# Performance work log

Hardware: AMD Instinct MI355X
Metric: run time of the kernel (lower is better)

Reference implementation:

```python
import jax, jax.numpy as jnp
import numpy as np

INPUT_DIM = 29
OUTPUT_DIM = 67
ES = 256
HS = 512
SRC_LEN = 64
TRG_LEN = 48
BATCH = 512


def _lstm_cell(x, h, c, Wih, Whh, bih, bhh):
    # PyTorch gate order: i, f, g, o
    g = x @ Wih.T + bih + h @ Whh.T + bhh
    i, f, gg, o = jnp.split(g, 4, axis=-1)
    c_new = jax.nn.sigmoid(f) * c + jax.nn.sigmoid(i) * jnp.tanh(gg)
    h_new = jax.nn.sigmoid(o) * jnp.tanh(c_new)
    return h_new, c_new


def setup_inputs() -> dict:
    key = jax.random.key(0)
    ks = jax.random.split(key, 32)
    s_es = 1.0 / np.sqrt(ES)
    s_hs = 1.0 / np.sqrt(HS)
    inp = {}
    inp['src'] = jax.random.randint(ks[0], (SRC_LEN, BATCH), 0, INPUT_DIM)
    inp['trg'] = jax.random.randint(ks[1], (TRG_LEN, BATCH), 0, OUTPUT_DIM)
    # encoder params
    inp['enc_emb'] = jax.random.normal(ks[2], (INPUT_DIM, ES), jnp.float32)
    inp['enc_Wih_f'] = jax.random.normal(ks[3], (4 * HS, ES), jnp.float32) * s_hs
    inp['enc_Whh_f'] = jax.random.normal(ks[4], (4 * HS, HS), jnp.float32) * s_hs
    inp['enc_bih_f'] = jax.random.normal(ks[5], (4 * HS,), jnp.float32) * s_hs
    inp['enc_bhh_f'] = jax.random.normal(ks[6], (4 * HS,), jnp.float32) * s_hs
    inp['enc_Wih_b'] = jax.random.normal(ks[7], (4 * HS, ES), jnp.float32) * s_hs
    inp['enc_Whh_b'] = jax.random.normal(ks[8], (4 * HS, HS), jnp.float32) * s_hs
    inp['enc_bih_b'] = jax.random.normal(ks[9], (4 * HS,), jnp.float32) * s_hs
    inp['enc_bhh_b'] = jax.random.normal(ks[10], (4 * HS,), jnp.float32) * s_hs
    inp['fc_h_W'] = jax.random.normal(ks[11], (HS, 2 * HS), jnp.float32) * s_hs
    inp['fc_h_b'] = jax.random.normal(ks[12], (HS,), jnp.float32) * s_hs
    inp['fc_c_W'] = jax.random.normal(ks[13], (HS, 2 * HS), jnp.float32) * s_hs
    inp['fc_c_b'] = jax.random.normal(ks[14], (HS,), jnp.float32) * s_hs
    # decoder params
    inp['dec_emb'] = jax.random.normal(ks[15], (OUTPUT_DIM, ES), jnp.float32)
    inp['dec_Wih'] = jax.random.normal(ks[16], (4 * HS, 2 * HS + ES), jnp.float32) * s_hs
    inp['dec_Whh'] = jax.random.normal(ks[17], (4 * HS, HS), jnp.float32) * s_hs
    inp['dec_bih'] = jax.random.normal(ks[18], (4 * HS,), jnp.float32) * s_hs
    inp['dec_bhh'] = jax.random.normal(ks[19], (4 * HS,), jnp.float32) * s_hs
    inp['energy_W'] = jax.random.normal(ks[20], (1, 3 * HS), jnp.float32) * s_hs
    inp['energy_b'] = jax.random.normal(ks[21], (1,), jnp.float32) * s_hs
    inp['fc_out_W'] = jax.random.normal(ks[22], (OUTPUT_DIM, HS), jnp.float32) * s_hs
    inp['fc_out_b'] = jax.random.normal(ks[23], (OUTPUT_DIM,), jnp.float32) * s_hs
    return inp


def _forward(src, trg, enc_emb, enc_Wih_f, enc_Whh_f, enc_bih_f, enc_bhh_f,
             enc_Wih_b, enc_Whh_b, enc_bih_b, enc_bhh_b,
             fc_h_W, fc_h_b, fc_c_W, fc_c_b,
             dec_emb, dec_Wih, dec_Whh, dec_bih, dec_bhh,
             energy_W, energy_b, fc_out_W, fc_out_b):
    S, B = src.shape
    T = trg.shape[0]
    emb = enc_emb[src]  # [S, B, ES]
    h0 = jnp.zeros((B, HS), emb.dtype)
    c0 = jnp.zeros((B, HS), emb.dtype)

    def fwd_step(carry, x_t):
        h, c = carry
        h, c = _lstm_cell(x_t, h, c, enc_Wih_f, enc_Whh_f, enc_bih_f, enc_bhh_f)
        return (h, c), h

    def bwd_step(carry, x_t):
        h, c = carry
        h, c = _lstm_cell(x_t, h, c, enc_Wih_b, enc_Whh_b, enc_bih_b, enc_bhh_b)
        return (h, c), h

    (hf, cf), out_f = jax.lax.scan(fwd_step, (h0, c0), emb)
    (hb, cb), out_b_rev = jax.lax.scan(bwd_step, (h0, c0), emb[::-1])
    out_b = out_b_rev[::-1]
    encoder_states = jnp.concatenate([out_f, out_b], axis=2)  # [S, B, 2H]

    # fc_h / fc_c compress the 2 directions' final hidden/cell to [B, H]
    hidden_h = jnp.concatenate([hf, hb], axis=-1) @ fc_h_W.T + fc_h_b
    hidden_c = jnp.concatenate([cf, cb], axis=-1) @ fc_c_W.T + fc_c_b

    # Attention: original code passes encoder_hidden on EVERY step, so the
    # attention weights and context vector are constant across decode steps.
    h_rep = jnp.broadcast_to(hidden_h[None], (S, B, HS))
    e_in = jnp.concatenate([h_rep, encoder_states], axis=2)  # [S, B, 3H]
    energy = jax.nn.relu(e_in @ energy_W.T + energy_b)  # [S, B, 1]
    attn = jax.nn.softmax(energy, axis=0)[..., 0]  # [S, B]
    context = jnp.einsum('sb,sbh->bh', attn, encoder_states)  # [B, 2H]

    # Decode: teacher_forcing_ratio = 1.0 -> inputs are trg[t-1]; since the
    # rnn initial state is reset to encoder_hidden each step, all T-1 steps
    # are independent and can be computed in parallel.
    dec_in_tok = trg[:-1]  # [T-1, B]
    emb_d = dec_emb[dec_in_tok]  # [T-1, B, ES]
    ctx_rep = jnp.broadcast_to(context[None], (T - 1, B, 2 * HS))
    rnn_in = jnp.concatenate([ctx_rep, emb_d], axis=2)  # [T-1, B, 2H+ES]
    h_new, _ = _lstm_cell(rnn_in, hidden_h[None], hidden_c[None],
                          dec_Wih, dec_Whh, dec_bih, dec_bhh)
    logits = h_new @ fc_out_W.T + fc_out_b  # [T-1, B, V]
    outputs = jnp.concatenate(
        [jnp.zeros((1, B, OUTPUT_DIM), logits.dtype), logits], axis=0)
    return outputs


def reference(src, trg, enc_emb, enc_Wih_f, enc_Whh_f, enc_bih_f, enc_bhh_f,
              enc_Wih_b, enc_Whh_b, enc_bih_b, enc_bhh_b,
              fc_h_W, fc_h_b, fc_c_W, fc_c_b,
              dec_emb, dec_Wih, dec_Whh, dec_bih, dec_bhh,
              energy_W, energy_b, fc_out_W, fc_out_b):
    return _forward(src, trg, enc_emb, enc_Wih_f, enc_Whh_f, enc_bih_f,
                    enc_bhh_f, enc_Wih_b, enc_Whh_b, enc_bih_b, enc_bhh_b,
                    fc_h_W, fc_h_b, fc_c_W, fc_c_b, dec_emb, dec_Wih,
                    dec_Whh, dec_bih, dec_bhh, energy_W, energy_b,
                    fc_out_W, fc_out_b)
```

## Files before the change

kernel.cpp:

```cpp
#include <hip/hip_runtime.h>
#include <cstddef>

#define BATCH 512
#define ESZ   256
#define HSZ   512
#define G4    2048
#define SRCL  64
#define TRGL  48
#define ODIM  67

typedef __bf16  bf8v    __attribute__((ext_vector_type(8)));
typedef float   floatx4 __attribute__((ext_vector_type(4)));

__device__ __forceinline__ float frcp(float x) { return __builtin_amdgcn_rcpf(x); }
__device__ __forceinline__ float fsig(float x) { return frcp(1.0f + __expf(-x)); }
__device__ __forceinline__ float ftanh(float x) { return 1.0f - 2.0f * frcp(1.0f + __expf(2.0f * x)); }

__global__ void embed_bf16(const int* __restrict__ tok, const float* __restrict__ table,
                           __bf16* __restrict__ out, int n_rows) {
    int i = blockIdx.x * 256 + threadIdx.x;
    int row = i >> 5;
    if (row >= n_rows) return;
    int e = (i & 31) << 3;
    const float* src = table + (size_t)tok[row] * ESZ + e;
    float4 a = *(const float4*)src;
    float4 b = *(const float4*)(src + 4);
    bf8v v;
    v[0] = (__bf16)a.x; v[1] = (__bf16)a.y; v[2] = (__bf16)a.z; v[3] = (__bf16)a.w;
    v[4] = (__bf16)b.x; v[5] = (__bf16)b.y; v[6] = (__bf16)b.z; v[7] = (__bf16)b.w;
    *(bf8v*)(out + (size_t)row * ESZ + e) = v;
}

__global__ void zero_kernel(float* __restrict__ p, int n) {
    int i = blockIdx.x * 256 + threadIdx.x;
    if (i < n) p[i] = 0.f;
}

__global__ void bias_prep(const float* __restrict__ af, const float* __restrict__ bf,
                          const float* __restrict__ ab, const float* __restrict__ bb,
                          const float* __restrict__ ad, const float* __restrict__ bd,
                          float* __restrict__ of, float* __restrict__ ob, float* __restrict__ od) {
    int i = blockIdx.x * 256 + threadIdx.x;
    if (i < G4) { of[i] = af[i] + bf[i]; ob[i] = ab[i] + bb[i]; od[i] = ad[i] + bd[i]; }
}

__device__ __forceinline__ bf8v cvt8(const float* __restrict__ s) {
    float4 a = *(const float4*)s;
    float4 b = *(const float4*)(s + 4);
    bf8v v;
    v[0] = (__bf16)a.x; v[1] = (__bf16)a.y; v[2] = (__bf16)a.z; v[3] = (__bf16)a.w;
    v[4] = (__bf16)b.x; v[5] = (__bf16)b.y; v[6] = (__bf16)b.z; v[7] = (__bf16)b.w;
    return v;
}

__global__ void wcat_bf16(const float* __restrict__ Wih, const float* __restrict__ Whh,
                          __bf16* __restrict__ Wc) {
    int i = blockIdx.x * 256 + threadIdx.x;
    int n = i / 96;
    int e = (i - n * 96) << 3;
    const float* src = (e < ESZ) ? (Wih + (size_t)n * ESZ + e)
                                 : (Whh + (size_t)n * HSZ + (e - ESZ));
    *(bf8v*)(Wc + (size_t)n * 768 + e) = cvt8(src);
}

__global__ void decw_bf16(const float* __restrict__ dec_Wih, __bf16* __restrict__ We) {
    int i = blockIdx.x * 256 + threadIdx.x;
    int n = i >> 5;
    int e = (i & 31) << 3;
    *(bf8v*)(We + (size_t)n * ESZ + e) =
        cvt8(dec_Wih + (size_t)n * (2 * HSZ + ESZ) + 2 * HSZ + e);
}

__global__ void wdcat_bf16(const float* __restrict__ dec_Wih, const float* __restrict__ dec_Whh,
                           __bf16* __restrict__ Wd) {
    int i = blockIdx.x * 256 + threadIdx.x;
    int n = i / 192;
    int e = (i - n * 192) << 3;
    const float* src = (e < 1024) ? (dec_Wih + (size_t)n * 1280 + e)
                                  : (dec_Whh + (size_t)n * HSZ + (e - 1024));
    *(bf8v*)(Wd + (size_t)n * 1536 + e) = cvt8(src);
}

__global__ void conv_f2b(const float* __restrict__ src, __bf16* __restrict__ dst, int n8) {
    int i = blockIdx.x * 256 + threadIdx.x;
    if (i < n8) *(bf8v*)(dst + (size_t)i * 8) = cvt8(src + (size_t)i * 8);
}

__global__ void fo_pad(const float* __restrict__ W, __bf16* __restrict__ dst) {
    int i = blockIdx.x * 256 + threadIdx.x;
    int r = i >> 6, e = (i & 63) << 3;
    bf8v v;
    if (r < ODIM) v = cvt8(W + (size_t)r * HSZ + e);
    else { for (int k = 0; k < 8; ++k) v[k] = (__bf16)0.f; }
    *(bf8v*)(dst + (size_t)r * HSZ + e) = v;
}

__global__ void cat_hfb(const __bf16* __restrict__ es, __bf16* __restrict__ dst) {
    int i = blockIdx.x * 256 + threadIdx.x;
    int r = i >> 7, e = (i & 127) << 3;
    const __bf16* s = (e < HSZ) ? (es + ((size_t)(63 * BATCH + r)) * 1024 + e)
                                : (es + (size_t)r * 1024 + e);
    *(bf8v*)(dst + (size_t)r * 1024 + e) = *(const bf8v*)s;
}

__global__ void cat_cfb(const float* __restrict__ cbuf, __bf16* __restrict__ dst) {
    int i = blockIdx.x * 256 + threadIdx.x;
    int r = i >> 7, e = (i & 127) << 3;
    const float* s = (e < HSZ) ? (cbuf + (size_t)r * HSZ + e)
                               : (cbuf + (size_t)BATCH * HSZ + (size_t)r * HSZ + (e - HSZ));
    *(bf8v*)(dst + (size_t)r * 1024 + e) = cvt8(s);
}

__global__ void cat_ctxh(const float* __restrict__ ctx, const float* __restrict__ hid_h,
                         __bf16* __restrict__ dst) {
    int i = blockIdx.x * 256 + threadIdx.x;
    int r = i / 192;
    int e = (i - r * 192) << 3;
    const float* s = (e < 1024) ? (ctx + (size_t)r * 1024 + e)
                                : (hid_h + (size_t)r * HSZ + (e - 1024));
    *(bf8v*)(dst + (size_t)r * 1536 + e) = cvt8(s);
}

__global__ __launch_bounds__(256) void enc_step_v3(
    const __bf16* __restrict__ embE, const __bf16* __restrict__ hPrev,
    __bf16* __restrict__ hNext, float* __restrict__ cbuf, __bf16* __restrict__ es,
    const __bf16* __restrict__ WcF, const __bf16* __restrict__ WcB,
    const float* __restrict__ biasF, const float* __restrict__ biasB, int t)
{
    __shared__ __bf16 As[64 * 136];
    __shared__ __bf16 Bs[64 * 136];
    __shared__ float  gbuf[64 * 64];

    const int dir = blockIdx.z;
    const int tt  = dir ? (SRCL - 1 - t) : t;
    const __bf16* Wc   = dir ? WcB : WcF;
    const float*  bias = dir ? biasB : biasF;
    const int j0 = blockIdx.x * 16;
    const int m0 = blockIdx.y * 64;

    const int tid = threadIdx.x;
    const int w = tid >> 6, lane = tid & 63;
    const int quad = lane >> 4, l15 = lane & 15;
    const int mh = (w & 1) * 32, gh = (w >> 1) * 32;

    floatx4 acc[2][2] = {};

    for (int p = 0; p < 6; ++p) {
        __syncthreads();
#pragma unroll
        for (int i = 0; i < 4; ++i) {
            int idx = tid + i * 256;
            int r = idx >> 4, kq = idx & 15;
            const __bf16* srcA;
            if (p < 2) srcA = embE + ((size_t)(tt * BATCH + m0 + r)) * ESZ + p * 128 + kq * 8;
            else       srcA = hPrev + ((size_t)(dir * BATCH + m0 + r)) * HSZ + (p - 2) * 128 + kq * 8;
            *(bf8v*)(As + r * 136 + kq * 8) = *(const bf8v*)srcA;
            int wrow = (r >> 4) * HSZ + j0 + (r & 15);
            *(bf8v*)(Bs + r * 136 + kq * 8) =
                *(const bf8v*)(Wc + (size_t)wrow * 768 + p * 128 + kq * 8);
        }
        __syncthreads();
#pragma unroll
        for (int ks = 0; ks < 4; ++ks) {
            int ko = (ks * 4 + quad) * 8;
            bf8v a0 = *(const bf8v*)(As + (mh + l15) * 136 + ko);
            bf8v a1 = *(const bf8v*)(As + (mh + 16 + l15) * 136 + ko);
            bf8v b0 = *(const bf8v*)(Bs + (gh + l15) * 136 + ko);
            bf8v b1 = *(const bf8v*)(Bs + (gh + 16 + l15) * 136 + ko);
            acc[0][0] = __builtin_amdgcn_mfma_f32_16x16x32_bf16(a0, b0, acc[0][0], 0, 0, 0);
            acc[0][1] = __builtin_amdgcn_mfma_f32_16x16x32_bf16(a0, b1, acc[0][1], 0, 0, 0);
            acc[1][0] = __builtin_amdgcn_mfma_f32_16x16x32_bf16(a1, b0, acc[1][0], 0, 0, 0);
            acc[1][1] = __builtin_amdgcn_mfma_f32_16x16x32_bf16(a1, b1, acc[1][1], 0, 0, 0);
        }
    }

#pragma unroll
    for (int ms = 0; ms < 2; ++ms)
#pragma unroll
        for (int cs = 0; cs < 2; ++cs)
#pragma unroll
            for (int r = 0; r < 4; ++r)
                gbuf[(mh + ms * 16 + quad * 4 + r) * 64 + gh + cs * 16 + l15] = acc[ms][cs][r];
    __syncthreads();

#pragma unroll
    for (int i = 0; i < 4; ++i) {
        int e = tid + i * 256;
        int m = e >> 4, jj = e & 15;
        float gi = gbuf[m * 64 + jj]      + bias[j0 + jj];
        float gf = gbuf[m * 64 + 16 + jj] + bias[HSZ + j0 + jj];
        float gg = gbuf[m * 64 + 32 + jj] + bias[2 * HSZ + j0 + jj];
        float go = gbuf[m * 64 + 48 + jj] + bias[3 * HSZ + j0 + jj];
        size_t ci = (size_t)(dir * BATCH + m0 + m) * HSZ + j0 + jj;
        float cn = fsig(gf) * cbuf[ci] + fsig(gi) * ftanh(gg);
        cbuf[ci] = cn;
        float hn = fsig(go) * ftanh(cn);
        hNext[ci] = (__bf16)hn;
        es[((size_t)(tt * BATCH + m0 + m)) * (2 * HSZ) + dir * HSZ + j0 + jj] = (__bf16)hn;
    }
}

__global__ __launch_bounds__(256) void gmm_bf16(
    const __bf16* __restrict__ A, const __bf16* __restrict__ B, int K,
    const float* __restrict__ bias, float* __restrict__ C, int ldc, int N)
{
    const int tid = threadIdx.x;
    const int w = tid >> 6, lane = tid & 63;
    const int quad = lane >> 4, l15 = lane & 15;
    const int n0 = blockIdx.x * 64;
    const int mA = blockIdx.y * 64 + w * 16 + l15;

    const __bf16* Ar = A + (size_t)mA * K + quad * 8;
    const __bf16* Br[4];
#pragma unroll
    for (int ns = 0; ns < 4; ++ns)
        Br[ns] = B + (size_t)(n0 + ns * 16 + l15) * K + quad * 8;

    floatx4 acc[4] = {};
    const int KT = K >> 5;
#pragma unroll 4
    for (int kt = 0; kt < KT; ++kt) {
        bf8v a = *(const bf8v*)(Ar + kt * 32);
#pragma unroll
        for (int ns = 0; ns < 4; ++ns) {
            bf8v b = *(const bf8v*)(Br[ns] + kt * 32);
            acc[ns] = __builtin_amdgcn_mfma_f32_16x16x32_bf16(a, b, acc[ns], 0, 0, 0);
        }
    }
    const int mb = blockIdx.y * 64 + w * 16 + quad * 4;
#pragma unroll
    for (int ns = 0; ns < 4; ++ns) {
        int n = n0 + ns * 16 + l15;
        if (n < N) {
#pragma unroll
            for (int r = 0; r < 4; ++r)
                C[(size_t)(mb + r) * ldc + n] = acc[ns][r] + bias[n];
        }
    }
}

__global__ __launch_bounds__(256) void dec_mfma(
    const __bf16* __restrict__ embD, const __bf16* __restrict__ We,
    const float* __restrict__ D0, const float* __restrict__ hidc,
    __bf16* __restrict__ h_new)
{
    const int tid = threadIdx.x;
    const int w = tid >> 6, lane = tid & 63;
    const int quad = lane >> 4, l15 = lane & 15;
    const int mA = blockIdx.y * 64 + w * 16 + l15;
    const int j0 = blockIdx.x * 32;

    const __bf16* Ar = embD + (size_t)mA * ESZ + quad * 8;
    const __bf16* Brow[4][2];
#pragma unroll
    for (int g = 0; g < 4; ++g)
#pragma unroll
        for (int ni = 0; ni < 2; ++ni)
            Brow[g][ni] = We + ((size_t)(g * HSZ + j0 + ni * 16 + l15)) * ESZ + quad * 8;

    floatx4 acc[4][2] = {};
#pragma unroll 4
    for (int kt = 0; kt < 8; ++kt) {
        bf8v a = *(const bf8v*)(Ar + kt * 32);
#pragma unroll
        for (int g = 0; g < 4; ++g)
#pragma unroll
            for (int ni = 0; ni < 2; ++ni) {
                bf8v b = *(const bf8v*)(Brow[g][ni] + kt * 32);
                acc[g][ni] = __builtin_amdgcn_mfma_f32_16x16x32_bf16(a, b, acc[g][ni], 0, 0, 0);
            }
    }

    const int mbase = blockIdx.y * 64 + w * 16 + quad * 4;
#pragma unroll
    for (int ni = 0; ni < 2; ++ni) {
        int j = j0 + ni * 16 + l15;
#pragma unroll
        for (int r = 0; r < 4; ++r) {
            int mr = mbase + r;
            int b = mr & (BATCH - 1);
            const float* d0 = D0 + (size_t)b * G4;
            float gi = acc[0][ni][r] + d0[j];
            float gf = acc[1][ni][r] + d0[HSZ + j];
            float gg = acc[2][ni][r] + d0[2 * HSZ + j];
            float go = acc[3][ni][r] + d0[3 * HSZ + j];
            float cn = fsig(gf) * hidc[(size_t)b * HSZ + j] + fsig(gi) * ftanh(gg);
            h_new[(size_t)mr * HSZ + j] = (__bf16)(fsig(go) * ftanh(cn));
        }
    }
}

__global__ void eh_kernel(const float* __restrict__ hid_h, const float* __restrict__ eW,
                          const float* __restrict__ eb, float* __restrict__ eh) {
    int w = blockIdx.x * 4 + (threadIdx.x >> 6);
    int lane = threadIdx.x & 63;
    if (w >= BATCH) return;
    float s = 0.f;
    for (int k = lane; k < HSZ; k += 64) s += hid_h[(size_t)w * HSZ + k] * eW[k];
    for (int off = 32; off; off >>= 1) s += __shfl_down(s, off);
    if (lane == 0) eh[w] = s + eb[0];
}

__global__ void energy_kernel(const __bf16* __restrict__ es, const float* __restrict__ eW2,
                              const float* __restrict__ eh, float* __restrict__ energy) {
    int w = blockIdx.x * 4 + (threadIdx.x >> 6);
    int lane = threadIdx.x & 63;
    int s = w >> 9, b = w & 511;
    const __bf16* row = es + ((size_t)s * BATCH + b) * (2 * HSZ);
    float v = 0.f;
    for (int k = lane; k < 2 * HSZ; k += 64) v += (float)row[k] * eW2[k];
    for (int off = 32; off; off >>= 1) v += __shfl_down(v, off);
    if (lane == 0) energy[(size_t)s * BATCH + b] = fmaxf(v + eh[b], 0.f);
}

__global__ void softmax_kernel(const float* __restrict__ energy, float* __restrict__ attn) {
    int b = blockIdx.x * 4 + (threadIdx.x >> 6);
    int lane = threadIdx.x & 63;
    if (b >= BATCH) return;
    float v = energy[(size_t)lane * BATCH + b];
    float m = v;
    for (int off = 32; off; off >>= 1) m = fmaxf(m, __shfl_xor(m, off));
    float e = __expf(v - m);
    float sum = e;
    for (int off = 32; off; off >>= 1) sum += __shfl_xor(sum, off);
    attn[(size_t)lane * BATCH + b] = e / sum;
}

__global__ void context_kernel(const float* __restrict__ attn, const __bf16* __restrict__ es,
                               float* __restrict__ ctx) {
    int b = blockIdx.x;
    int j = threadIdx.x * 4;
    float a0 = 0.f, a1 = 0.f, a2 = 0.f, a3 = 0.f;
    for (int s = 0; s < SRCL; ++s) {
        float a = attn[(size_t)s * BATCH + b];
        const __bf16* r = es + ((size_t)s * BATCH + b) * (2 * HSZ) + j;
        a0 += a * (float)r[0]; a1 += a * (float)r[1];
        a2 += a * (float)r[2]; a3 += a * (float)r[3];
    }
    float4 o = make_float4(a0, a1, a2, a3);
    *(float4*)(ctx + (size_t)b * (2 * HSZ) + j) = o;
}

extern "C" void kernel_launch(void* const* d_in, const int* in_sizes, int n_in,
                              void* d_out, int out_size, void* d_ws, size_t ws_size,
                              hipStream_t stream) {
    const int*   src      = (const int*)d_in[0];
    const int*   trg      = (const int*)d_in[1];
    const float* enc_emb  = (const float*)d_in[2];
    const float* Wih_f    = (const float*)d_in[3];
    const float* Whh_f    = (const float*)d_in[4];
    const float* bih_f    = (const float*)d_in[5];
    const float* bhh_f    = (const float*)d_in[6];
    const float* Wih_b    = (const float*)d_in[7];
    const float* Whh_b    = (const float*)d_in[8];
    const float* bih_b    = (const float*)d_in[9];
    const float* bhh_b    = (const float*)d_in[10];
    const float* fc_h_W   = (const float*)d_in[11];
    const float* fc_h_b   = (const float*)d_in[12];
    const float* fc_c_W   = (const float*)d_in[13];
    const float* fc_c_b   = (const float*)d_in[14];
    const float* dec_emb  = (const float*)d_in[15];
    const float* dec_Wih  = (const float*)d_in[16];
    const float* dec_Whh  = (const float*)d_in[17];
    const float* dec_bih  = (const float*)d_in[18];
    const float* dec_bhh  = (const float*)d_in[19];
    const float* energy_W = (const float*)d_in[20];
    const float* energy_b = (const float*)d_in[21];
    const float* fc_out_W = (const float*)d_in[22];
    const float* fc_out_b = (const float*)d_in[23];
    float* out = (float*)d_out;

    float* ws = (float*)d_ws;
    size_t o = 0;
    __bf16* embE = (__bf16*)(ws + o); o += 4194304;
    __bf16* embD = (__bf16*)(ws + o); o += 3080192;
    __bf16* es   = (__bf16*)(ws + o); o += 16777216;
    float* zbase = ws + o;
    __bf16* h0   = (__bf16*)(ws + o); o += 262144;
    __bf16* h1   = (__bf16*)(ws + o); o += 262144;
    float*  cbuf = ws + o;            o += 524288;
    __bf16* WcF  = (__bf16*)(ws + o); o += 786432;
    __bf16* WcB  = (__bf16*)(ws + o); o += 786432;
    __bf16* decWe= (__bf16*)(ws + o); o += 262144;
    __bf16* WdC  = (__bf16*)(ws + o); o += 1572864;
    __bf16* fcWh = (__bf16*)(ws + o); o += 262144;
    __bf16* fcWc = (__bf16*)(ws + o); o += 262144;
    __bf16* foWb = (__bf16*)(ws + o); o += 32768;
    __bf16* hfb  = (__bf16*)(ws + o); o += 262144;
    __bf16* cfb  = (__bf16*)(ws + o); o += 262144;
    __bf16* ctxh = (__bf16*)(ws + o); o += 393216;
    float* hid_h = ws + o;            o += 262144;
    float* hid_c = ws + o;            o += 262144;
    float* ehv   = ws + o;            o += 512;
    float* energy= ws + o;            o += 32768;
    float* attn  = ws + o;            o += 32768;
    float* ctx   = ws + o;            o += 524288;
    float* D0    = ws + o;            o += 1048576;
    float* bias_f= ws + o;            o += 2048;
    float* bias_b= ws + o;            o += 2048;
    float* bias_d= ws + o;            o += 2048;
    __bf16* h_new= (__bf16*)(ws + o); o += 6160384;

    embed_bf16<<<4096, 256, 0, stream>>>(src, enc_emb, embE, SRCL * BATCH);
    embed_bf16<<<3008, 256, 0, stream>>>(trg, dec_emb, embD, (TRGL - 1) * BATCH);
    zero_kernel<<<4096, 256, 0, stream>>>(zbase, 1048576);
    bias_prep<<<8, 256, 0, stream>>>(bih_f, bhh_f, bih_b, bhh_b, dec_bih, dec_bhh,
                                     bias_f, bias_b, bias_d);
    wcat_bf16<<<768, 256, 0, stream>>>(Wih_f, Whh_f, WcF);
    wcat_bf16<<<768, 256, 0, stream>>>(Wih_b, Whh_b, WcB);
    decw_bf16<<<256, 256, 0, stream>>>(dec_Wih, decWe);
    wdcat_bf16<<<1536, 256, 0, stream>>>(dec_Wih, dec_Whh, WdC);
    conv_f2b<<<256, 256, 0, stream>>>(fc_h_W, fcWh, 65536);
    conv_f2b<<<256, 256, 0, stream>>>(fc_c_W, fcWc, 65536);
    fo_pad<<<32, 256, 0, stream>>>(fc_out_W, foWb);

    for (int t = 0; t < SRCL; ++t) {
        const __bf16* hp = (t & 1) ? h1 : h0;
        __bf16*       hn = (t & 1) ? h0 : h1;
        enc_step_v3<<<dim3(32, 8, 2), 256, 0, stream>>>(
            embE, hp, hn, cbuf, es, WcF, WcB, bias_f, bias_b, t);
    }

    cat_hfb<<<256, 256, 0, stream>>>(es, hfb);
    cat_cfb<<<256, 256, 0, stream>>>(cbuf, cfb);
    gmm_bf16<<<dim3(8, 8), 256, 0, stream>>>(hfb, fcWh, 1024, fc_h_b, hid_h, HSZ, HSZ);
    gmm_bf16<<<dim3(8, 8), 256, 0, stream>>>(cfb, fcWc, 1024, fc_c_b, hid_c, HSZ, HSZ);

    eh_kernel<<<128, 256, 0, stream>>>(hid_h, energy_W, energy_b, ehv);
    energy_kernel<<<8192, 256, 0, stream>>>(es, energy_W + HSZ, ehv, energy);
    softmax_kernel<<<128, 256, 0, stream>>>(energy, attn);
    context_kernel<<<512, 256, 0, stream>>>(attn, es, ctx);

    cat_ctxh<<<384, 256, 0, stream>>>(ctx, hid_h, ctxh);
    gmm_bf16<<<dim3(32, 8), 256, 0, stream>>>(ctxh, WdC, 1536, bias_d, D0, G4, G4);

    dec_mfma<<<dim3(16, 376), 256, 0, stream>>>(embD, decWe, D0, hid_c, h_new);

    zero_kernel<<<134, 256, 0, stream>>>(out, BATCH * ODIM);
    gmm_bf16<<<dim3(2, 376), 256, 0, stream>>>(h_new, foWb, HSZ, fc_out_b,
                                               out + (size_t)BATCH * ODIM, ODIM, ODIM);
}
```

Measured before the change: 1.315 ms.

## Fuse encoder timesteps into a persistent kernel with grid barriers; retile decoder

Replaces the 64 per-timestep encoder launches with one persistent kernel of 256 blocks. Each block keeps its slice of the recurrent weights resident in shared memory and synchronises only with the 16 blocks sharing its batch rows through atomic counters between timesteps. The decoder gate kernel is also retiled to 128-row tiles staged in LDS, reading a gate-interleaved copy of D0 produced by a new swizzle kernel. The persistent kernel removes launch overhead and repeated weight reloads, but it requires all 256 blocks to be co-resident (launch_bounds 256,1) and adds spin-wait barrier latency on every step.

```diff
diff --git a/kernel.cpp b/kernel.cpp
--- a/kernel.cpp
+++ b/kernel.cpp
@@ -11,6 +11,10 @@
 
 typedef __bf16  bf8v    __attribute__((ext_vector_type(8)));
 typedef float   floatx4 __attribute__((ext_vector_type(4)));
+
+__device__ __forceinline__ floatx4 MF(bf8v a, bf8v b, floatx4 c) {
+    return __builtin_amdgcn_mfma_f32_16x16x32_bf16(a, b, c, 0, 0, 0);
+}
 
 __device__ __forceinline__ float frcp(float x) { return __builtin_amdgcn_rcpf(x); }
 __device__ __forceinline__ float fsig(float x) { return frcp(1.0f + __expf(-x)); }
@@ -121,82 +125,193 @@
     *(bf8v*)(dst + (size_t)r * 1536 + e) = cvt8(s);
 }
 
-__global__ __launch_bounds__(256) void enc_step_v3(
-    const __bf16* __restrict__ embE, const __bf16* __restrict__ hPrev,
-    __bf16* __restrict__ hNext, float* __restrict__ cbuf, __bf16* __restrict__ es,
+__global__ void d0_swz(const float* __restrict__ D0, float* __restrict__ D0s) {
+    int i = blockIdx.x * 256 + threadIdx.x;
+    int b = i >> 11, rest = i & 2047, g = rest >> 9, j = rest & 511;
+    D0s[(((size_t)b * 512 + j) << 2) + g] = D0[i];
+}
+
+#define ENC_STRIDE 520
+__global__ __launch_bounds__(256, 1) void enc_scan(
+    const __bf16* __restrict__ embE,
+    __bf16* __restrict__ h0, __bf16* __restrict__ h1,
+    float* __restrict__ cbuf, __bf16* __restrict__ es,
     const __bf16* __restrict__ WcF, const __bf16* __restrict__ WcB,
-    const float* __restrict__ biasF, const float* __restrict__ biasB, int t)
+    const float* __restrict__ biasF, const float* __restrict__ biasB,
+    unsigned int* __restrict__ cnt)
 {
-    __shared__ __bf16 As[64 * 136];
-    __shared__ __bf16 Bs[64 * 136];
-    __shared__ float  gbuf[64 * 64];
-
-    const int dir = blockIdx.z;
-    const int tt  = dir ? (SRCL - 1 - t) : t;
+    __shared__ __bf16 Bs[128 * ENC_STRIDE];
+
+    const int bid = blockIdx.x;
+    const int dir = bid >> 7;
+    const int rem = bid & 127;
+    const int m0  = (rem >> 4) * 64;
+    const int j0  = (rem & 15) * 32;
+    const int grp = bid >> 4;
+
     const __bf16* Wc   = dir ? WcB : WcF;
     const float*  bias = dir ? biasB : biasF;
-    const int j0 = blockIdx.x * 16;
-    const int m0 = blockIdx.y * 64;
-
+
+    const int tid  = threadIdx.x;
+    const int w    = tid >> 6, lane = tid & 63;
+    const int quad = lane >> 4, l15 = lane & 15;
+    const int mh   = (w & 1) * 32;
+    const int ghi  = w >> 1;
+    const int jl   = l15 + ghi * 16;
+
+#pragma unroll 4
+    for (int i = 0; i < 32; ++i) {
+        int idx = tid + i * 256;
+        int r = idx >> 6, ch = idx & 63;
+        int gate = (r >> 4) & 3;
+        int jr = (r & 15) + ((r >> 6) << 4);
+        *(bf8v*)(&Bs[r * ENC_STRIDE + ch * 8]) =
+            *(const bf8v*)(Wc + (size_t)(gate * HSZ + j0 + jr) * 768 + 256 + ch * 8);
+    }
+
+    const __bf16* BxP[4];
+    float bsv[4];
+#pragma unroll
+    for (int g = 0; g < 4; ++g) {
+        BxP[g] = Wc + (size_t)(g * HSZ + j0 + jl) * 768 + quad * 8;
+        bsv[g] = bias[g * HSZ + j0 + jl];
+    }
+
+    const size_t dirb = (size_t)dir * BATCH * HSZ;
+    const __bf16* BhBase = &Bs[(ghi * 64 + l15) * ENC_STRIDE + quad * 8];
+    __syncthreads();
+
+    for (int t = 0; t < SRCL; ++t) {
+        const int tt = dir ? (SRCL - 1 - t) : t;
+        const __bf16* hp = (t & 1) ? h1 : h0;
+        __bf16*       hn = (t & 1) ? h0 : h1;
+
+        floatx4 acc[2][4] = {};
+
+        const __bf16* Ax = embE + ((size_t)tt * BATCH + m0 + mh + l15) * ESZ + quad * 8;
+#pragma unroll 4
+        for (int kt = 0; kt < 8; ++kt) {
+            bf8v a0 = *(const bf8v*)(Ax + kt * 32);
+            bf8v a1 = *(const bf8v*)(Ax + 16 * ESZ + kt * 32);
+#pragma unroll
+            for (int g = 0; g < 4; ++g) {
+                bf8v b = *(const bf8v*)(BxP[g] + kt * 32);
+                acc[0][g] = MF(a0, b, acc[0][g]);
+                acc[1][g] = MF(a1, b, acc[1][g]);
+            }
+        }
+        const __bf16* Ah = hp + dirb + (size_t)(m0 + mh + l15) * HSZ + quad * 8;
+#pragma unroll 4
+        for (int kt = 0; kt < 16; ++kt) {
+            bf8v a0 = *(const bf8v*)(Ah + kt * 32);
+            bf8v a1 = *(const bf8v*)(Ah + 16 * HSZ + kt * 32);
+#pragma unroll
+            for (int g = 0; g < 4; ++g) {
+                bf8v b = *(const bf8v*)(BhBase + g * 16 * ENC_STRIDE + kt * 32);
+                acc[0][g] = MF(a0, b, acc[0][g]);
+                acc[1][g] = MF(a1, b, acc[1][g]);
+            }
+        }
+
+        const int j = j0 + jl;
+#pragma unroll
+        for (int ms = 0; ms < 2; ++ms) {
+            int mr = m0 + mh + ms * 16 + quad * 4;
+#pragma unroll
+            for (int r = 0; r < 4; ++r) {
+                int m = mr + r;
+                float gi = acc[ms][0][r] + bsv[0];
+                float gf = acc[ms][1][r] + bsv[1];
+                float gg = acc[ms][2][r] + bsv[2];
+                float go = acc[ms][3][r] + bsv[3];
+                size_t ci = dirb + (size_t)m * HSZ + j;
+                float cn = fsig(gf) * cbuf[ci] + fsig(gi) * ftanh(gg);
+                cbuf[ci] = cn;
+                float hv = fsig(go) * ftanh(cn);
+                hn[ci] = (__bf16)hv;
+                es[((size_t)tt * BATCH + m) * (2 * HSZ) + dir * HSZ + j] = (__bf16)hv;
+            }
+        }
+
+        if (t != SRCL - 1) {
+            __threadfence();
+            __syncthreads();
+            if (tid == 0) {
+                unsigned int* c = cnt + t * 16 + grp;
+                atomicAdd(c, 1u);
+                while (__hip_atomic_load(c, __ATOMIC_RELAXED, __HIP_MEMORY_SCOPE_AGENT) < 16u)
+                    __builtin_amdgcn_s_sleep(8);
+            }
+            __syncthreads();
+            __threadfence();
+        }
+    }
+}
+
+#define DA_STR 264
+__global__ __launch_bounds__(256) void dec_v4(
+    const __bf16* __restrict__ embD, const __bf16* __restrict__ We,
+    const float* __restrict__ D0s, const float* __restrict__ hidc,
+    __bf16* __restrict__ h_new)
+{
+    __shared__ __bf16 As[128 * DA_STR];
+    __shared__ __bf16 Bs2[128 * DA_STR];
+
+    const int m0 = blockIdx.y * 128;
+    const int j0 = blockIdx.x * 32;
     const int tid = threadIdx.x;
     const int w = tid >> 6, lane = tid & 63;
     const int quad = lane >> 4, l15 = lane & 15;
-    const int mh = (w & 1) * 32, gh = (w >> 1) * 32;
-
-    floatx4 acc[2][2] = {};
-
-    for (int p = 0; p < 6; ++p) {
-        __syncthreads();
-#pragma unroll
-        for (int i = 0; i < 4; ++i) {
-            int idx = tid + i * 256;
-            int r = idx >> 4, kq = idx & 15;
-            const __bf16* srcA;
-            if (p < 2) srcA = embE + ((size_t)(tt * BATCH + m0 + r)) * ESZ + p * 128 + kq * 8;
-            else       srcA = hPrev + ((size_t)(dir * BATCH + m0 + r)) * HSZ + (p - 2) * 128 + kq * 8;
-            *(bf8v*)(As + r * 136 + kq * 8) = *(const bf8v*)srcA;
-            int wrow = (r >> 4) * HSZ + j0 + (r & 15);
-            *(bf8v*)(Bs + r * 136 + kq * 8) =
-                *(const bf8v*)(Wc + (size_t)wrow * 768 + p * 128 + kq * 8);
-        }
-        __syncthreads();
-#pragma unroll
-        for (int ks = 0; ks < 4; ++ks) {
-            int ko = (ks * 4 + quad) * 8;
-            bf8v a0 = *(const bf8v*)(As + (mh + l15) * 136 + ko);
-            bf8v a1 = *(const bf8v*)(As + (mh + 16 + l15) * 136 + ko);
-            bf8v b0 = *(const bf8v*)(Bs + (gh + l15) * 136 + ko);
-            bf8v b1 = *(const bf8v*)(Bs + (gh + 16 + l15) * 136 + ko);
-            acc[0][0] = __builtin_amdgcn_mfma_f32_16x16x32_bf16(a0, b0, acc[0][0], 0, 0, 0);
-            acc[0][1] = __builtin_amdgcn_mfma_f32_16x16x32_bf16(a0, b1, acc[0][1], 0, 0, 0);
-            acc[1][0] = __builtin_amdgcn_mfma_f32_16x16x32_bf16(a1, b0, acc[1][0], 0, 0, 0);
-            acc[1][1] = __builtin_amdgcn_mfma_f32_16x16x32_bf16(a1, b1, acc[1][1], 0, 0, 0);
-        }
-    }
-
-#pragma unroll
-    for (int ms = 0; ms < 2; ++ms)
-#pragma unroll
-        for (int cs = 0; cs < 2; ++cs)
-#pragma unroll
-            for (int r = 0; r < 4; ++r)
-                gbuf[(mh + ms * 16 + quad * 4 + r) * 64 + gh + cs * 16 + l15] = acc[ms][cs][r];
+    const int mh = (w & 1) * 64;
+    const int ghi = w >> 1;
+    const int jl = l15 + ghi * 16;
+
+#pragma unroll 4
+    for (int i = 0; i < 16; ++i) {
+        int idx = tid + i * 256;
+        int r = idx >> 5, ch = idx & 31;
+        *(bf8v*)(&As[r * DA_STR + ch * 8]) =
+            *(const bf8v*)(embD + (size_t)(m0 + r) * ESZ + ch * 8);
+        int gate = (r >> 4) & 3;
+        int jr = (r & 15) + ((r >> 6) << 4);
+        *(bf8v*)(&Bs2[r * DA_STR + ch * 8]) =
+            *(const bf8v*)(We + (size_t)(gate * HSZ + j0 + jr) * ESZ + ch * 8);
+    }
     __syncthreads();
 
-#pragma unroll
-    for (int i = 0; i < 4; ++i) {
-        int e = tid + i * 256;
-        int m = e >> 4, jj = e & 15;
-        float gi = gbuf[m * 64 + jj]      + bias[j0 + jj];
-        float gf = gbuf[m * 64 + 16 + jj] + bias[HSZ + j0 + jj];
-        float gg = gbuf[m * 64 + 32 + jj] + bias[2 * HSZ + j0 + jj];
-        float go = gbuf[m * 64 + 48 + jj] + bias[3 * HSZ + j0 + jj];
-        size_t ci = (size_t)(dir * BATCH + m0 + m) * HSZ + j0 + jj;
-        float cn = fsig(gf) * cbuf[ci] + fsig(gi) * ftanh(gg);
-        cbuf[ci] = cn;
-        float hn = fsig(go) * ftanh(cn);
-        hNext[ci] = (__bf16)hn;
-        es[((size_t)(tt * BATCH + m0 + m)) * (2 * HSZ) + dir * HSZ + j0 + jj] = (__bf16)hn;
+    floatx4 acc[4][4] = {};
+    const __bf16* BhB = &Bs2[(ghi * 64 + l15) * DA_STR + quad * 8];
+#pragma unroll 4
+    for (int kt = 0; kt < 8; ++kt) {
+        bf8v a[4];
+#pragma unroll
+        for (int ms = 0; ms < 4; ++ms)
+            a[ms] = *(const bf8v*)(&As[(mh + ms * 16 + l15) * DA_STR + quad * 8 + kt * 32]);
+#pragma unroll
+        for (int g = 0; g < 4; ++g) {
+            bf8v b = *(const bf8v*)(BhB + g * 16 * DA_STR + kt * 32);
+#pragma unroll
+            for (int ms = 0; ms < 4; ++ms)
+                acc[ms][g] = MF(a[ms], b, acc[ms][g]);
+        }
+    }
+
+    const int j = j0 + jl;
+#pragma unroll
+    for (int ms = 0; ms < 4; ++ms) {
+        int mr = m0 + mh + ms * 16 + quad * 4;
+#pragma unroll
+        for (int r = 0; r < 4; ++r) {
+            int m = mr + r;
+            int b = m & (BATCH - 1);
+            floatx4 d0 = *(const floatx4*)(D0s + (((size_t)b * 512 + j) << 2));
+            float gi = acc[ms][0][r] + d0[0];
+            float gf = acc[ms][1][r] + d0[1];
+            float gg = acc[ms][2][r] + d0[2];
+            float go = acc[ms][3][r] + d0[3];
+            float cn = fsig(gf) * hidc[(size_t)b * HSZ + j] + fsig(gi) * ftanh(gg);
+            h_new[(size_t)m * HSZ + j] = (__bf16)(fsig(go) * ftanh(cn));
+        }
     }
 }
 
@@ -224,7 +339,7 @@
 #pragma unroll
         for (int ns = 0; ns < 4; ++ns) {
             bf8v b = *(const bf8v*)(Br[ns] + kt * 32);
-            acc[ns] = __builtin_amdgcn_mfma_f32_16x16x32_bf16(a, b, acc[ns], 0, 0, 0);
+            acc[ns] = MF(a, b, acc[ns]);
         }
     }
     const int mb = blockIdx.y * 64 + w * 16 + quad * 4;
@@ -235,57 +350,6 @@
 #pragma unroll
             for (int r = 0; r < 4; ++r)
                 C[(size_t)(mb + r) * ldc + n] = acc[ns][r] + bias[n];
-        }
-    }
-}
-
-__global__ __launch_bounds__(256) void dec_mfma(
-    const __bf16* __restrict__ embD, const __bf16* __restrict__ We,
-    const float* __restrict__ D0, const float* __restrict__ hidc,
-    __bf16* __restrict__ h_new)
-{
-    const int tid = threadIdx.x;
-    const int w = tid >> 6, lane = tid & 63;
-    const int quad = lane >> 4, l15 = lane & 15;
-    const int mA = blockIdx.y * 64 + w * 16 + l15;
-    const int j0 = blockIdx.x * 32;
-
-    const __bf16* Ar = embD + (size_t)mA * ESZ + quad * 8;
-    const __bf16* Brow[4][2];
-#pragma unroll
-    for (int g = 0; g < 4; ++g)
-#pragma unroll
-        for (int ni = 0; ni < 2; ++ni)
-            Brow[g][ni] = We + ((size_t)(g * HSZ + j0 + ni * 16 + l15)) * ESZ + quad * 8;
-
-    floatx4 acc[4][2] = {};
-#pragma unroll 4
-    for (int kt = 0; kt < 8; ++kt) {
-        bf8v a = *(const bf8v*)(Ar + kt * 32);
-#pragma unroll
-        for (int g = 0; g < 4; ++g)
-#pragma unroll
-            for (int ni = 0; ni < 2; ++ni) {
-                bf8v b = *(const bf8v*)(Brow[g][ni] + kt * 32);
-                acc[g][ni] = __builtin_amdgcn_mfma_f32_16x16x32_bf16(a, b, acc[g][ni], 0, 0, 0);
-            }
-    }
-
-    const int mbase = blockIdx.y * 64 + w * 16 + quad * 4;
-#pragma unroll
-    for (int ni = 0; ni < 2; ++ni) {
-        int j = j0 + ni * 16 + l15;
-#pragma unroll
-        for (int r = 0; r < 4; ++r) {
-            int mr = mbase + r;
-            int b = mr & (BATCH - 1);
-            const float* d0 = D0 + (size_t)b * G4;
-            float gi = acc[0][ni][r] + d0[j];
-            float gf = acc[1][ni][r] + d0[HSZ + j];
-            float gg = acc[2][ni][r] + d0[2 * HSZ + j];
-            float go = acc[3][ni][r] + d0[3 * HSZ + j];
-            float cn = fsig(gf) * hidc[(size_t)b * HSZ + j] + fsig(gi) * ftanh(gg);
-            h_new[(size_t)mr * HSZ + j] = (__bf16)(fsig(go) * ftanh(cn));
         }
     }
 }
@@ -396,14 +460,17 @@
     float* attn  = ws + o;            o += 32768;
     float* ctx   = ws + o;            o += 524288;
     float* D0    = ws + o;            o += 1048576;
+    float* D0s   = ws + o;            o += 1048576;
     float* bias_f= ws + o;            o += 2048;
     float* bias_b= ws + o;            o += 2048;
     float* bias_d= ws + o;            o += 2048;
     __bf16* h_new= (__bf16*)(ws + o); o += 6160384;
+    unsigned int* cnt = (unsigned int*)(ws + o); o += 1024;
 
     embed_bf16<<<4096, 256, 0, stream>>>(src, enc_emb, embE, SRCL * BATCH);
     embed_bf16<<<3008, 256, 0, stream>>>(trg, dec_emb, embD, (TRGL - 1) * BATCH);
     zero_kernel<<<4096, 256, 0, stream>>>(zbase, 1048576);
+    zero_kernel<<<4, 256, 0, stream>>>((float*)cnt, 1024);
     bias_prep<<<8, 256, 0, stream>>>(bih_f, bhh_f, bih_b, bhh_b, dec_bih, dec_bhh,
                                      bias_f, bias_b, bias_d);
     wcat_bf16<<<768, 256, 0, stream>>>(Wih_f, Whh_f, WcF);
@@ -414,12 +481,8 @@
     conv_f2b<<<256, 256, 0, stream>>>(fc_c_W, fcWc, 65536);
     fo_pad<<<32, 256, 0, stream>>>(fc_out_W, foWb);
 
-    for (int t = 0; t < SRCL; ++t) {
-        const __bf16* hp = (t & 1) ? h1 : h0;
-        __bf16*       hn = (t & 1) ? h0 : h1;
-        enc_step_v3<<<dim3(32, 8, 2), 256, 0, stream>>>(
-            embE, hp, hn, cbuf, es, WcF, WcB, bias_f, bias_b, t);
-    }
+    enc_scan<<<256, 256, 0, stream>>>(embE, h0, h1, cbuf, es, WcF, WcB,
+                                      bias_f, bias_b, cnt);
 
     cat_hfb<<<256, 256, 0, stream>>>(es, hfb);
     cat_cfb<<<256, 256, 0, stream>>>(cbuf, cfb);
@@ -433,8 +496,9 @@
 
     cat_ctxh<<<384, 256, 0, stream>>>(ctx, hid_h, ctxh);
     gmm_bf16<<<dim3(32, 8), 256, 0, stream>>>(ctxh, WdC, 1536, bias_d, D0, G4, G4);
-
-    dec_mfma<<<dim3(16, 376), 256, 0, stream>>>(embD, decWe, D0, hid_c, h_new);
+    d0_swz<<<4096, 256, 0, stream>>>(D0, D0s);
+
+    dec_v4<<<dim3(16, 188), 256, 0, stream>>>(embD, decWe, D0s, hid_c, h_new);
 
     zero_kernel<<<134, 256, 0, stream>>>(out, BATCH * ODIM);
     gmm_bf16<<<dim3(2, 376), 256, 0, stream>>>(h_new, foWb, HSZ, fc_out_b,
```

New measurement: 5.217 ms. 297% more time.
